# Kernel optimization log

Hardware: AMD Instinct MI355X
Metric: run time of the kernel (lower is better)

## Reference

```python
import jax, jax.numpy as jnp
import numpy as np

B, C, D, H, W = 2, 64, 8, 24, 24  # hidden_dim = C; N = D*H*W = 4608 tokens


def setup_inputs() -> dict:
    key = jax.random.key(0)
    ks = jax.random.split(key, 8)
    s = 1.0 / np.sqrt(C)  # fan-in style init for 1x1 conv weights
    return {
        "x": jax.random.normal(ks[0], (B, C, D, H, W), dtype=jnp.float32),
        "h": jax.random.normal(ks[1], (B, C, D, H, W), dtype=jnp.float32),
        "Wq": jax.random.normal(ks[2], (C, C), dtype=jnp.float32) * s,
        "bq": jax.random.normal(ks[3], (C,), dtype=jnp.float32) * s,
        "Wk": jax.random.normal(ks[4], (C, C), dtype=jnp.float32) * s,
        "bk": jax.random.normal(ks[5], (C,), dtype=jnp.float32) * s,
        "Wv": jax.random.normal(ks[6], (C, C), dtype=jnp.float32) * s,
        "bv": jax.random.normal(ks[7], (C,), dtype=jnp.float32) * s,
    }


def reference(x, h, Wq, bq, Wk, bk, Wv, bv):
    # 1x1 Conv3d == per-token linear over channels
    def proj(inp, Wt, bt):
        f = inp.reshape(inp.shape[0], inp.shape[1], -1)  # [B, C, N]
        return jnp.einsum('oc,bcn->bon', Wt, f) + bt[None, :, None]

    q = proj(x, Wq, bq)  # [B, C, N]
    k = proj(h, Wk, bk)  # [B, C, N]
    v = proj(h, Wv, bv)  # [B, C, N]

    scale = 1.0 / np.sqrt(k.shape[1])  # k.size(1) ** 0.5 == sqrt(C)
    scores = jnp.einsum('bcm,bcn->bmn', q, k) * scale  # [B, N, N]
    attn = jax.nn.softmax(scores, axis=-1)
    out = jnp.einsum('bcn,bmn->bcm', v, attn)  # [B, C, N]
    return out.reshape(h.shape)
```

## Files before the change

kernel.cpp:

```cpp
#include <hip/hip_runtime.h>
#include <hip/hip_bf16.h>

#define C_DIM 64
#define N_TOK 4608
#define NBLK  72
#define B_SZ  2
#define MBLKS 144
#define NSEG  8
#define SEGLEN (N_TOK / NSEG)
#define KTILES 288
#define VTILES 72
#define OSTR  68

typedef __bf16 bf16x8 __attribute__((ext_vector_type(8)));
typedef float  f32x4  __attribute__((ext_vector_type(4)));


__device__ __forceinline__ void gemm_tile(
    const __hip_bfloat16* wmat, const bf16x8 bin[2], const float* bias,
    int col, int quad, f32x4 acc[4])
{
    #pragma unroll
    for (int ot = 0; ot < 4; ot++) {
        f32x4 a = (f32x4){0.f, 0.f, 0.f, 0.f};
        #pragma unroll
        for (int kh = 0; kh < 2; kh++) {
            bf16x8 wf = *(const bf16x8*)(wmat + (ot * 16 + col) * 72 +
                                         kh * 32 + quad * 8);
            a = __builtin_amdgcn_mfma_f32_16x16x32_bf16(wf, bin[kh], a, 0, 0, 0);
        }
        float4 b4 = *(const float4*)(bias + ot * 16 + quad * 4);
        a[0] += b4.x; a[1] += b4.y; a[2] += b4.z; a[3] += b4.w;
        acc[ot] = a;
    }
}

__global__ __launch_bounds__(256) void proj_kernel(
    const float* __restrict__ x,  const float* __restrict__ h,
    const float* __restrict__ Wq, const float* __restrict__ bq,
    const float* __restrict__ Wk, const float* __restrict__ bk,
    const float* __restrict__ Wv, const float* __restrict__ bv,
    __hip_bfloat16* __restrict__ qS, __hip_bfloat16* __restrict__ kS,
    __hip_bfloat16* __restrict__ vS)
{
    __shared__ __hip_bfloat16 wl[3 * 64 * 72];
    __shared__ __hip_bfloat16 xt[64 * 72];
    __shared__ __hip_bfloat16 ht[64 * 72];
    __shared__ __hip_bfloat16 vl[64 * 72];

    const int b  = blockIdx.x / NBLK;
    const int n0 = (blockIdx.x % NBLK) * 64;
    const int t  = threadIdx.x;

    #pragma unroll
    for (int mat = 0; mat < 3; mat++) {
        const float* W = (mat == 0) ? Wq : ((mat == 1) ? Wk : Wv);
        __hip_bfloat16* wd = wl + mat * (64 * 72);
        #pragma unroll
        for (int i = 0; i < 4; i++) {
            const int ch = i * 256 + t;
            const int o = ch >> 4, c0 = (ch & 15) * 4;
            float4 w4 = *(const float4*)(W + ch * 4);
            union { __hip_bfloat16 e[4]; uint2 v; } pk;
            pk.e[0] = __float2bfloat16(w4.x); pk.e[1] = __float2bfloat16(w4.y);
            pk.e[2] = __float2bfloat16(w4.z); pk.e[3] = __float2bfloat16(w4.w);
            *(uint2*)(wd + o * 72 + c0) = pk.v;
        }
    }
    #pragma unroll
    for (int i = 0; i < 4; i++) {
        const int ch = i * 256 + t;
        const int c = ch >> 4, n4 = (ch & 15) * 4;
        float4 x4 = *(const float4*)(x + (size_t)(b * C_DIM + c) * N_TOK + n0 + n4);
        float4 h4 = *(const float4*)(h + (size_t)(b * C_DIM + c) * N_TOK + n0 + n4);
        xt[(n4 + 0) * 72 + c] = __float2bfloat16(x4.x);
        xt[(n4 + 1) * 72 + c] = __float2bfloat16(x4.y);
        xt[(n4 + 2) * 72 + c] = __float2bfloat16(x4.z);
        xt[(n4 + 3) * 72 + c] = __float2bfloat16(x4.w);
        ht[(n4 + 0) * 72 + c] = __float2bfloat16(h4.x);
        ht[(n4 + 1) * 72 + c] = __float2bfloat16(h4.y);
        ht[(n4 + 2) * 72 + c] = __float2bfloat16(h4.z);
        ht[(n4 + 3) * 72 + c] = __float2bfloat16(h4.w);
    }
    __syncthreads();

    const int wave = t >> 6, lane = t & 63;
    const int col = lane & 15, quad = lane >> 4;

    bf16x8 xb[2], hb[2];
    #pragma unroll
    for (int kh = 0; kh < 2; kh++) {
        xb[kh] = *(const bf16x8*)(xt + (wave * 16 + col) * 72 + kh * 32 + quad * 8);
        hb[kh] = *(const bf16x8*)(ht + (wave * 16 + col) * 72 + kh * 32 + quad * 8);
    }

    f32x4 acc[4];

    gemm_tile(wl + 0 * (64 * 72), xb, bq, col, quad, acc);
    {
        const size_t tile16 = (size_t)b * KTILES + (n0 >> 4) + wave;
        const float SC = 0.125f * 1.44269504088896f;
        #pragma unroll
        for (int ot = 0; ot < 4; ot++) {
            union { __hip_bfloat16 e[4]; uint2 v; } pk;
            #pragma unroll
            for (int r = 0; r < 4; r++) pk.e[r] = __float2bfloat16(acc[ot][r] * SC);
            *(uint2*)(qS + (tile16 << 10) + (ot >> 1) * 512 +
                      ((ot * 2 + (quad >> 1)) & 3) * 128 + col * 8 +
                      (quad & 1) * 4) = pk.v;
        }
    }

    gemm_tile(wl + 1 * (64 * 72), hb, bk, col, quad, acc);
    {
        const int t_l = (wave >> 1) * 2 + ((col >> 2) & 1);
        const int row = ((wave * 2 + (col >> 3)) & 3) * 4 + (col & 3);
        const size_t tile16 = (size_t)b * KTILES + (n0 >> 4) + t_l;
        #pragma unroll
        for (int ot = 0; ot < 4; ot++) {
            union { __hip_bfloat16 e[4]; uint2 v; } pk;
            #pragma unroll
            for (int r = 0; r < 4; r++) pk.e[r] = __float2bfloat16(acc[ot][r]);
            *(uint2*)(kS + (tile16 << 10) + (ot >> 1) * 512 +
                      ((ot * 2 + (quad >> 1)) & 3) * 128 + row * 8 +
                      (quad & 1) * 4) = pk.v;
        }
    }

    gemm_tile(wl + 2 * (64 * 72), hb, bv, col, quad, acc);
    #pragma unroll
    for (int ot = 0; ot < 4; ot++)
        #pragma unroll
        for (int r = 0; r < 4; r++)
            vl[(ot * 16 + quad * 4 + r) * 72 + wave * 16 + col] =
                __float2bfloat16(acc[ot][r]);
    __syncthreads();
    {
        const size_t vbase = ((size_t)(b * VTILES) + (n0 >> 6)) << 12;
        #pragma unroll
        for (int rep = 0; rep < 2; rep++) {
            const int ch = rep * 256 + t;
            const int cc = ch >> 7, hf = (ch >> 6) & 1;
            const int qd = (ch >> 4) & 3, c2 = ch & 15;
            *(uint4*)(vS + vbase + (size_t)ch * 8) =
                *(const uint4*)(vl + (cc * 16 + c2) * 72 + hf * 32 + qd * 8);
        }
    }
}

__global__ __launch_bounds__(512) void attn_kernel(
    const __hip_bfloat16* __restrict__ qS,
    const __hip_bfloat16* __restrict__ kS,
    const __hip_bfloat16* __restrict__ vS,
    float* __restrict__ out)
{
    __shared__ float o_lds[NSEG * 16 * OSTR];
    __shared__ float lstat[NSEG][32];

    const int b    = blockIdx.x / MBLKS;
    const int mblk = blockIdx.x % MBLKS;
    const int wave = threadIdx.x >> 6;
    const int lane = threadIdx.x & 63;
    const int col  = lane & 15;
    const int quad = lane >> 4;
    const int m0   = mblk * 32;

    const __hip_bfloat16* qp =
        qS + (((size_t)b * KTILES + (m0 >> 4)) << 10) + lane * 8;
    const bf16x8 qa0 = *(const bf16x8*)(qp);
    const bf16x8 qa1 = *(const bf16x8*)(qp + 512);
    const bf16x8 qb0 = *(const bf16x8*)(qp + 1024);
    const bf16x8 qb1 = *(const bf16x8*)(qp + 1536);

    f32x4 accO0[4], accO1[4];
    #pragma unroll
    for (int cc = 0; cc < 4; cc++) {
        accO0[cc] = (f32x4){0.f, 0.f, 0.f, 0.f};
        accO1[cc] = (f32x4){0.f, 0.f, 0.f, 0.f};
    }
    float rsum0 = 0.f, rsum1 = 0.f;

    const int nbeg = wave * SEGLEN;

    #pragma unroll 1
    for (int n0 = nbeg; n0 < nbeg + SEGLEN; n0 += 64) {
        const __hip_bfloat16* kt =
            kS + (((size_t)b * KTILES + (n0 >> 4)) << 10) + lane * 8;
        bf16x8 ka[8];
        #pragma unroll
        for (int j = 0; j < 4; j++) {
            ka[2 * j]     = *(const bf16x8*)(kt + (j << 10));
            ka[2 * j + 1] = *(const bf16x8*)(kt + (j << 10) + 512);
        }
        const __hip_bfloat16* vt =
            vS + ((((size_t)b * VTILES) + (n0 >> 6)) << 12) + lane * 8;
        bf16x8 va[8];
        #pragma unroll
        for (int cc = 0; cc < 4; cc++) {
            va[2 * cc]     = *(const bf16x8*)(vt + cc * 1024);
            va[2 * cc + 1] = *(const bf16x8*)(vt + cc * 1024 + 512);
        }

        f32x4 s0[4], s1[4];
        #pragma unroll
        for (int j = 0; j < 4; j++) {
            s0[j] = __builtin_amdgcn_mfma_f32_16x16x32_bf16(
                        ka[2 * j], qa0, (f32x4){0.f, 0.f, 0.f, 0.f}, 0, 0, 0);
            s0[j] = __builtin_amdgcn_mfma_f32_16x16x32_bf16(ka[2 * j + 1], qa1, s0[j], 0, 0, 0);
            s1[j] = __builtin_amdgcn_mfma_f32_16x16x32_bf16(
                        ka[2 * j], qb0, (f32x4){0.f, 0.f, 0.f, 0.f}, 0, 0, 0);
            s1[j] = __builtin_amdgcn_mfma_f32_16x16x32_bf16(ka[2 * j + 1], qb1, s1[j], 0, 0, 0);
        }

        union { __hip_bfloat16 e[8]; bf16x8 v; } p00, p01, p10, p11;
        #pragma unroll
        for (int j = 0; j < 2; j++)
            #pragma unroll
            for (int r = 0; r < 4; r++) {
                float e0 = __builtin_amdgcn_exp2f(s0[j][r]);
                float e1 = __builtin_amdgcn_exp2f(s0[2 + j][r]);
                rsum0 += e0 + e1;
                p00.e[j * 4 + r] = __float2bfloat16(e0);
                p01.e[j * 4 + r] = __float2bfloat16(e1);
                float f0 = __builtin_amdgcn_exp2f(s1[j][r]);
                float f1 = __builtin_amdgcn_exp2f(s1[2 + j][r]);
                rsum1 += f0 + f1;
                p10.e[j * 4 + r] = __float2bfloat16(f0);
                p11.e[j * 4 + r] = __float2bfloat16(f1);
            }

        #pragma unroll
        for (int cc = 0; cc < 4; cc++) {
            accO0[cc] = __builtin_amdgcn_mfma_f32_16x16x32_bf16(va[2 * cc],     p00.v, accO0[cc], 0, 0, 0);
            accO0[cc] = __builtin_amdgcn_mfma_f32_16x16x32_bf16(va[2 * cc + 1], p01.v, accO0[cc], 0, 0, 0);
            accO1[cc] = __builtin_amdgcn_mfma_f32_16x16x32_bf16(va[2 * cc],     p10.v, accO1[cc], 0, 0, 0);
            accO1[cc] = __builtin_amdgcn_mfma_f32_16x16x32_bf16(va[2 * cc + 1], p11.v, accO1[cc], 0, 0, 0);
        }
    }

    rsum0 += __shfl_xor(rsum0, 16);  rsum0 += __shfl_xor(rsum0, 32);
    rsum1 += __shfl_xor(rsum1, 16);  rsum1 += __shfl_xor(rsum1, 32);
    if (quad == 0) {
        lstat[wave][col]      = rsum0;
        lstat[wave][16 + col] = rsum1;
    }

    #pragma unroll
    for (int phase = 0; phase < 2; phase++) {
        const f32x4* accp = phase ? accO1 : accO0;
        #pragma unroll
        for (int cc = 0; cc < 4; cc++)
            *(f32x4*)(o_lds + (wave * 16 + col) * OSTR + cc * 16 + quad * 4) =
                accp[cc];
        __syncthreads();
        if (threadIdx.x < 256) {
            const int m  = threadIdx.x & 15;
            const int cq = threadIdx.x >> 4;
            const int mi = phase * 16 + m;
            float lsum = 0.f;
            f32x4 oacc = (f32x4){0.f, 0.f, 0.f, 0.f};
            #pragma unroll
            for (int sgm = 0; sgm < NSEG; sgm++) {
                lsum += lstat[sgm][mi];
                oacc += *(const f32x4*)(o_lds + (sgm * 16 + m) * OSTR + cq * 4);
            }
            const float inv = 1.0f / lsum;
            #pragma unroll
            for (int r = 0; r < 4; r++) {
                const int c = cq * 4 + r;
                out[(size_t)(b * C_DIM + c) * N_TOK + m0 + phase * 16 + m] =
                    oacc[r] * inv;
            }
        }
        __syncthreads();
    }
}

extern "C" void kernel_launch(void* const* d_in, const int* in_sizes, int n_in,
                              void* d_out, int out_size, void* d_ws, size_t ws_size,
                              hipStream_t stream) {
    const float* x  = (const float*)d_in[0];
    const float* h  = (const float*)d_in[1];
    const float* Wq = (const float*)d_in[2];
    const float* bq = (const float*)d_in[3];
    const float* Wk = (const float*)d_in[4];
    const float* bk = (const float*)d_in[5];
    const float* Wv = (const float*)d_in[6];
    const float* bv = (const float*)d_in[7];
    float* out = (float*)d_out;

    const size_t elems = (size_t)B_SZ * N_TOK * C_DIM;
    __hip_bfloat16* qS = (__hip_bfloat16*)d_ws;
    __hip_bfloat16* kS = qS + elems;
    __hip_bfloat16* vS = kS + elems;

    proj_kernel<<<B_SZ * NBLK, 256, 0, stream>>>(x, h, Wq, bq, Wk, bk, Wv, bv,
                                                 qS, kS, vS);
    attn_kernel<<<B_SZ * MBLKS, 512, 0, stream>>>(qS, kS, vS, out);
}
```

Baseline: 105.2 us.

## Process 64 queries per attention block to reuse K/V tiles across four subtiles

Each attention block now handles 64 query rows (four 16-row subtiles) instead of 32, so each K and V tile loaded into registers is used by four MFMA groups. This reduces K/V load traffic per query and halves the grid size. It increases accumulator register pressure and leaves fewer blocks than compute units, which risks idle CUs and lower occupancy.

Measured after the change: 93.52 us, median of 2. -11.1%, faster.

```diff
diff --git a/kernel.cpp b/kernel.cpp
--- a/kernel.cpp
+++ b/kernel.cpp
@@ -5,7 +5,7 @@
 #define N_TOK 4608
 #define NBLK  72
 #define B_SZ  2
-#define MBLKS 144
+#define M64BLKS 72
 #define NSEG  8
 #define SEGLEN (N_TOK / NSEG)
 #define KTILES 288
@@ -155,30 +155,32 @@
     float* __restrict__ out)
 {
     __shared__ float o_lds[NSEG * 16 * OSTR];
-    __shared__ float lstat[NSEG][32];
-
-    const int b    = blockIdx.x / MBLKS;
-    const int mblk = blockIdx.x % MBLKS;
+    __shared__ float lstat[NSEG][64];
+
+    const int b    = blockIdx.x / M64BLKS;
+    const int mblk = blockIdx.x % M64BLKS;
     const int wave = threadIdx.x >> 6;
     const int lane = threadIdx.x & 63;
     const int col  = lane & 15;
     const int quad = lane >> 4;
-    const int m0   = mblk * 32;
+    const int m0   = mblk * 64;
 
     const __hip_bfloat16* qp =
         qS + (((size_t)b * KTILES + (m0 >> 4)) << 10) + lane * 8;
-    const bf16x8 qa0 = *(const bf16x8*)(qp);
-    const bf16x8 qa1 = *(const bf16x8*)(qp + 512);
-    const bf16x8 qb0 = *(const bf16x8*)(qp + 1024);
-    const bf16x8 qb1 = *(const bf16x8*)(qp + 1536);
-
-    f32x4 accO0[4], accO1[4];
-    #pragma unroll
-    for (int cc = 0; cc < 4; cc++) {
-        accO0[cc] = (f32x4){0.f, 0.f, 0.f, 0.f};
-        accO1[cc] = (f32x4){0.f, 0.f, 0.f, 0.f};
-    }
-    float rsum0 = 0.f, rsum1 = 0.f;
+    bf16x8 qa[4][2];
+    #pragma unroll
+    for (int ms = 0; ms < 4; ms++) {
+        qa[ms][0] = *(const bf16x8*)(qp + ms * 1024);
+        qa[ms][1] = *(const bf16x8*)(qp + ms * 1024 + 512);
+    }
+
+    f32x4 accO[4][4];
+    #pragma unroll
+    for (int ms = 0; ms < 4; ms++)
+        #pragma unroll
+        for (int cc = 0; cc < 4; cc++)
+            accO[ms][cc] = (f32x4){0.f, 0.f, 0.f, 0.f};
+    float rsum[4] = {0.f, 0.f, 0.f, 0.f};
 
     const int nbeg = wave * SEGLEN;
 
@@ -201,57 +203,55 @@
             va[2 * cc + 1] = *(const bf16x8*)(vt + cc * 1024 + 512);
         }
 
-        f32x4 s0[4], s1[4];
-        #pragma unroll
-        for (int j = 0; j < 4; j++) {
-            s0[j] = __builtin_amdgcn_mfma_f32_16x16x32_bf16(
-                        ka[2 * j], qa0, (f32x4){0.f, 0.f, 0.f, 0.f}, 0, 0, 0);
-            s0[j] = __builtin_amdgcn_mfma_f32_16x16x32_bf16(ka[2 * j + 1], qa1, s0[j], 0, 0, 0);
-            s1[j] = __builtin_amdgcn_mfma_f32_16x16x32_bf16(
-                        ka[2 * j], qb0, (f32x4){0.f, 0.f, 0.f, 0.f}, 0, 0, 0);
-            s1[j] = __builtin_amdgcn_mfma_f32_16x16x32_bf16(ka[2 * j + 1], qb1, s1[j], 0, 0, 0);
-        }
-
-        union { __hip_bfloat16 e[8]; bf16x8 v; } p00, p01, p10, p11;
-        #pragma unroll
-        for (int j = 0; j < 2; j++)
-            #pragma unroll
-            for (int r = 0; r < 4; r++) {
-                float e0 = __builtin_amdgcn_exp2f(s0[j][r]);
-                float e1 = __builtin_amdgcn_exp2f(s0[2 + j][r]);
-                rsum0 += e0 + e1;
-                p00.e[j * 4 + r] = __float2bfloat16(e0);
-                p01.e[j * 4 + r] = __float2bfloat16(e1);
-                float f0 = __builtin_amdgcn_exp2f(s1[j][r]);
-                float f1 = __builtin_amdgcn_exp2f(s1[2 + j][r]);
-                rsum1 += f0 + f1;
-                p10.e[j * 4 + r] = __float2bfloat16(f0);
-                p11.e[j * 4 + r] = __float2bfloat16(f1);
+        #pragma unroll
+        for (int ms = 0; ms < 4; ms++) {
+            f32x4 s[4];
+            #pragma unroll
+            for (int j = 0; j < 4; j++) {
+                s[j] = __builtin_amdgcn_mfma_f32_16x16x32_bf16(
+                           ka[2 * j], qa[ms][0], (f32x4){0.f, 0.f, 0.f, 0.f}, 0, 0, 0);
+                s[j] = __builtin_amdgcn_mfma_f32_16x16x32_bf16(
+                           ka[2 * j + 1], qa[ms][1], s[j], 0, 0, 0);
             }
-
-        #pragma unroll
-        for (int cc = 0; cc < 4; cc++) {
-            accO0[cc] = __builtin_amdgcn_mfma_f32_16x16x32_bf16(va[2 * cc],     p00.v, accO0[cc], 0, 0, 0);
-            accO0[cc] = __builtin_amdgcn_mfma_f32_16x16x32_bf16(va[2 * cc + 1], p01.v, accO0[cc], 0, 0, 0);
-            accO1[cc] = __builtin_amdgcn_mfma_f32_16x16x32_bf16(va[2 * cc],     p10.v, accO1[cc], 0, 0, 0);
-            accO1[cc] = __builtin_amdgcn_mfma_f32_16x16x32_bf16(va[2 * cc + 1], p11.v, accO1[cc], 0, 0, 0);
-        }
-    }
-
-    rsum0 += __shfl_xor(rsum0, 16);  rsum0 += __shfl_xor(rsum0, 32);
-    rsum1 += __shfl_xor(rsum1, 16);  rsum1 += __shfl_xor(rsum1, 32);
+            union { __hip_bfloat16 e[8]; bf16x8 v; } p0, p1;
+            float ps = 0.f;
+            #pragma unroll
+            for (int j = 0; j < 2; j++)
+                #pragma unroll
+                for (int r = 0; r < 4; r++) {
+                    float e0 = __builtin_amdgcn_exp2f(s[j][r]);
+                    float e1 = __builtin_amdgcn_exp2f(s[2 + j][r]);
+                    ps += e0 + e1;
+                    p0.e[j * 4 + r] = __float2bfloat16(e0);
+                    p1.e[j * 4 + r] = __float2bfloat16(e1);
+                }
+            rsum[ms] += ps;
+            #pragma unroll
+            for (int cc = 0; cc < 4; cc++) {
+                accO[ms][cc] = __builtin_amdgcn_mfma_f32_16x16x32_bf16(
+                                   va[2 * cc], p0.v, accO[ms][cc], 0, 0, 0);
+                accO[ms][cc] = __builtin_amdgcn_mfma_f32_16x16x32_bf16(
+                                   va[2 * cc + 1], p1.v, accO[ms][cc], 0, 0, 0);
+            }
+        }
+    }
+
+    #pragma unroll
+    for (int ms = 0; ms < 4; ms++) {
+        rsum[ms] += __shfl_xor(rsum[ms], 16);
+        rsum[ms] += __shfl_xor(rsum[ms], 32);
+    }
     if (quad == 0) {
-        lstat[wave][col]      = rsum0;
-        lstat[wave][16 + col] = rsum1;
-    }
-
-    #pragma unroll
-    for (int phase = 0; phase < 2; phase++) {
-        const f32x4* accp = phase ? accO1 : accO0;
+        #pragma unroll
+        for (int ms = 0; ms < 4; ms++) lstat[wave][ms * 16 + col] = rsum[ms];
+    }
+
+    #pragma unroll
+    for (int phase = 0; phase < 4; phase++) {
         #pragma unroll
         for (int cc = 0; cc < 4; cc++)
             *(f32x4*)(o_lds + (wave * 16 + col) * OSTR + cc * 16 + quad * 4) =
-                accp[cc];
+                accO[phase][cc];
         __syncthreads();
         if (threadIdx.x < 256) {
             const int m  = threadIdx.x & 15;
@@ -296,5 +296,5 @@
 
     proj_kernel<<<B_SZ * NBLK, 256, 0, stream>>>(x, h, Wq, bq, Wk, bk, Wv, bv,
                                                  qS, kS, vS);
-    attn_kernel<<<B_SZ * MBLKS, 512, 0, stream>>>(qS, kS, vS, out);
+    attn_kernel<<<B_SZ * M64BLKS, 512, 0, stream>>>(qS, kS, vS, out);
 }
```
